# Kernel optimization log

Hardware: AMD Instinct MI355X
Metric: run time of the kernel (lower is better)

The kernel has to match this reference:

```python
import jax, jax.numpy as jnp
import numpy as np

B, S, H = 4, 2048, 2048
E, K = 4, 2
FF = 4 * H  # standard MLP expert expansion


def setup_inputs() -> dict:
    key = jax.random.key(0)
    ks = jax.random.split(key, 5)
    sc = 0.02
    return {
        "hidden_states": jax.random.normal(ks[0], (B, S, H), jnp.float32),
        "w_gate": jax.random.normal(ks[1], (H, E), jnp.float32) * sc,
        "b_gate": jnp.zeros((E,), jnp.float32),
        "w1": jax.random.normal(ks[2], (E, H, FF), jnp.float32) * sc,
        "b1": jnp.zeros((E, FF), jnp.float32),
        "w2": jax.random.normal(ks[3], (E, FF, H), jnp.float32) * sc,
        "b2": jnp.zeros((E, H), jnp.float32),
    }


def reference(hidden_states, w_gate, b_gate, w1, b1, w2, b2):
    # Router: linear gate -> softmax -> top-k, renormalized gate weights
    logits = jnp.einsum("bsh,he->bse", hidden_states, w_gate) + b_gate
    probs = jax.nn.softmax(logits, axis=-1)                       # [B,S,E]
    top_p, top_i = jax.lax.top_k(probs, K)                        # [B,S,K]
    gate_w = top_p / jnp.sum(top_p, axis=-1, keepdims=True)

    # Switch-style load-balancing aux loss
    route = jax.nn.one_hot(top_i, E, dtype=probs.dtype)           # [B,S,K,E]
    frac_tokens = jnp.mean(jnp.sum(route, axis=2) / K, axis=(0, 1))  # [E]
    mean_prob = jnp.mean(probs, axis=(0, 1))                      # [E]
    aux_loss = E * jnp.sum(frac_tokens * mean_prob)

    # Dispatch/combine: small fixed expert count -> loop over experts,
    # dense FFN on all tokens, mask via gate weight (0 for unrouted tokens).
    out = jnp.zeros_like(hidden_states)
    for e in range(E):
        w_e = jnp.sum(gate_w * (top_i == e), axis=-1)             # [B,S]
        h = jax.nn.gelu(jnp.einsum("bsh,hf->bsf", hidden_states, w1[e]) + b1[e])
        y = jnp.einsum("bsf,fh->bsh", h, w2[e]) + b2[e]
        out = out + w_e[..., None] * y
    return out, aux_loss
```

## Files before the change

### kernel.cpp

```cpp
#include <hip/hip_runtime.h>

typedef unsigned short u16;
typedef __attribute__((ext_vector_type(8))) short bf16x8;
typedef __attribute__((ext_vector_type(4))) float f32x4;

#define TOK  8192
#define HD   2048
#define FFD  8192
#define NEXP 4
#define CAPE 4352

__device__ __forceinline__ u16 f2bf(float f){
  unsigned u = __float_as_uint(f);
  u += 0x7fffu + ((u >> 16) & 1u);
  return (u16)(u >> 16);
}

__device__ __forceinline__ float gelu_tanh(float x){
  float u = 0.7978845608028654f * (x + 0.044715f * x * x * x);
  return 0.5f * x * (1.0f + tanhf(u));
}

__device__ __forceinline__ void gload_lds16(const void* g, void* l){
  __builtin_amdgcn_global_load_lds((const __attribute__((address_space(1))) void*)g,
                                   (__attribute__((address_space(3))) void*)l, 16, 0, 0);
}

__device__ __forceinline__ f32x4 mfma_bf16(bf16x8 a, bf16x8 b, f32x4 c){
  asm("v_mfma_f32_16x16x32_bf16 %0, %1, %2, %0" : "+v"(c) : "v"(a), "v"(b));
  return c;
}

__global__ __launch_bounds__(256) void cvt_to_bf16(const float* __restrict__ in,
                                                   u16* __restrict__ out, int n4){
  int i = blockIdx.x * 256 + threadIdx.x;
  if (i >= n4) return;
  float4 v = ((const float4*)in)[i];
  ushort4 o;
  o.x = f2bf(v.x); o.y = f2bf(v.y); o.z = f2bf(v.z); o.w = f2bf(v.w);
  ((ushort4*)out)[i] = o;
}

__global__ __launch_bounds__(256) void transpose_cvt(const float* __restrict__ in,
                                                     u16* __restrict__ out, int R, int C){
  __shared__ u16 t[64][138];
  const int tx = threadIdx.x & 63;
  const int w  = threadIdx.x >> 6;
  const size_t r0 = (size_t)blockIdx.y * 128;
  const size_t c0 = (size_t)blockIdx.x * 64;
  #pragma unroll
  for (int i = 0; i < 32; i++){
    const int r = w * 32 + i;
    t[tx][r] = f2bf(in[(r0 + r) * C + c0 + tx]);
  }
  __syncthreads();
  #pragma unroll
  for (int j = 0; j < 16; j++){
    const int c = j * 4 + w;
    ushort2 o;
    o.x = t[c][2 * tx];
    o.y = t[c][2 * tx + 1];
    *(ushort2*)(out + (c0 + c) * (size_t)R + r0 + 2 * tx) = o;
  }
}

__global__ __launch_bounds__(256) void router_kernel(
    const float* __restrict__ X, const float* __restrict__ wg, const float* __restrict__ bg,
    float* __restrict__ probs, int* __restrict__ topi, float* __restrict__ gatew){
  int t = blockIdx.x;
  const float* x = X + (size_t)t * HD;
  float a0 = 0.f, a1 = 0.f, a2 = 0.f, a3 = 0.f;
  for (int h = threadIdx.x; h < HD; h += 256){
    float xv = x[h];
    float4 w = ((const float4*)wg)[h];
    a0 += xv * w.x; a1 += xv * w.y; a2 += xv * w.z; a3 += xv * w.w;
  }
  __shared__ float red[4][256];
  red[0][threadIdx.x] = a0; red[1][threadIdx.x] = a1;
  red[2][threadIdx.x] = a2; red[3][threadIdx.x] = a3;
  __syncthreads();
  for (int s = 128; s > 0; s >>= 1){
    if (threadIdx.x < (unsigned)s){
      #pragma unroll
      for (int e = 0; e < 4; e++) red[e][threadIdx.x] += red[e][threadIdx.x + s];
    }
    __syncthreads();
  }
  if (threadIdx.x == 0){
    float l[4], p[4];
    #pragma unroll
    for (int e = 0; e < 4; e++) l[e] = red[e][0] + bg[e];
    float mx = fmaxf(fmaxf(l[0], l[1]), fmaxf(l[2], l[3]));
    float s = 0.f;
    #pragma unroll
    for (int e = 0; e < 4; e++){ p[e] = expf(l[e] - mx); s += p[e]; }
    #pragma unroll
    for (int e = 0; e < 4; e++){ p[e] /= s; probs[t * 4 + e] = p[e]; }
    int e0 = 0;
    for (int e = 1; e < 4; e++) if (p[e] > p[e0]) e0 = e;
    int e1 = -1;
    for (int e = 0; e < 4; e++){ if (e == e0) continue; if (e1 < 0 || p[e] > p[e1]) e1 = e; }
    float g = p[e0] + p[e1];
    topi[t * 2] = e0; topi[t * 2 + 1] = e1;
    #pragma unroll
    for (int e = 0; e < 4; e++)
      gatew[(size_t)e * TOK + t] = (e == e0) ? p[e0] / g : (e == e1) ? p[e1] / g : 0.f;
  }
}

__global__ __launch_bounds__(256) void build_lists(const int* __restrict__ topi,
                                                   int* __restrict__ cnt,
                                                   int* __restrict__ lists){
  int t = blockIdx.x * 256 + threadIdx.x;
  if (t >= TOK) return;
  #pragma unroll
  for (int k = 0; k < 2; k++){
    int e = topi[t * 2 + k];
    int p = atomicAdd(cnt + e, 1);
    lists[e * TOK + p] = t;
  }
}

__global__ __launch_bounds__(256) void aux_kernel(const float* __restrict__ probs,
                                                  const int* __restrict__ topi,
                                                  float* __restrict__ out_aux){
  __shared__ float sp[4][256];
  __shared__ float sc[4][256];
  float p[4] = {0,0,0,0}, c[4] = {0,0,0,0};
  for (int t = threadIdx.x; t < TOK; t += 256){
    #pragma unroll
    for (int e = 0; e < 4; e++) p[e] += probs[t * 4 + e];
    c[topi[t * 2]]     += 1.f;
    c[topi[t * 2 + 1]] += 1.f;
  }
  #pragma unroll
  for (int e = 0; e < 4; e++){ sp[e][threadIdx.x] = p[e]; sc[e][threadIdx.x] = c[e]; }
  __syncthreads();
  for (int s = 128; s > 0; s >>= 1){
    if (threadIdx.x < (unsigned)s){
      #pragma unroll
      for (int e = 0; e < 4; e++){
        sp[e][threadIdx.x] += sp[e][threadIdx.x + s];
        sc[e][threadIdx.x] += sc[e][threadIdx.x + s];
      }
    }
    __syncthreads();
  }
  if (threadIdx.x == 0){
    float aux = 0.f;
    #pragma unroll
    for (int e = 0; e < 4; e++)
      aux += (sc[e][0] / (float)(TOK * 2)) * (sp[e][0] / (float)TOK);
    *out_aux = 4.f * aux;
  }
}

template<int EPI, int N, int K>
__global__ __launch_bounds__(256) void gemm_97(
    const u16* __restrict__ A, const u16* __restrict__ BT,
    const int* __restrict__ rowidx, const int* __restrict__ cntp,
    const float* __restrict__ bias,
    u16* __restrict__ Hout,
    const float* __restrict__ gate, float* __restrict__ Cout)
{
  __shared__ __align__(16) u16 As[128 * 64];
  __shared__ __align__(16) u16 Bs[128 * 64];
  const int Mv = *cntp;
  const int gx = gridDim.x, gy = gridDim.y;
  const int orig = blockIdx.x + gx * blockIdx.y;
  const int xcd = orig & 7, rank = orig >> 3;
  const int bxl = rank / gy, by = rank % gy;
  const int bx = xcd * (gx >> 3) + bxl;
  const int browg = by * 128;
  if (browg >= Mv) return;
  const size_t bcol = (size_t)bx * 128;

  const int tid = threadIdx.x, lane = tid & 63, w = tid >> 6;
  const int wr = w >> 1, wc = w & 1;
  const int l8 = lane >> 3;
  const int csw  = ((lane & 7) ^ l8) * 8;
  const int sw   = (lane & 7) * 8;
  const int h8   = ((lane >> 4) & 3) * 8;
  const int colk0 = h8 ^ sw, colk1 = (32 | h8) ^ sw;
  const int r16 = lane & 15;

  const u16* bsrc[4]; int bch[4];
  #pragma unroll
  for (int j = 0; j < 4; j++){
    int rb = j * 32 + w * 8;
    bch[j] = rb * 128;
    bsrc[j] = BT + (bcol + rb + l8) * (size_t)K + csw;
  }
  const u16* asrc[4]; int ach[4];
  #pragma unroll
  for (int q = 0; q < 4; q++){
    int rb = wr * 64 + q * 16 + wc * 8;
    ach[q] = rb * 128;
    int rl = browg + rb + l8;
    int ar;
    if (EPI == 0){
      if (rl > Mv - 1) rl = Mv - 1;
      ar = rowidx[rl];
    } else {
      ar = rl;
    }
    asrc[q] = A + (size_t)ar * K + csw;
  }

  f32x4 acc[4][4];
  #pragma unroll
  for (int m = 0; m < 4; m++)
    #pragma unroll
    for (int n = 0; n < 4; n++) acc[m][n] = (f32x4){0.f, 0.f, 0.f, 0.f};
  bf16x8 bC[8];

  const int NT = K / 64;
  for (int t = 0; t < NT; ++t){
    const size_t ko = (size_t)t * 64;
    __syncthreads();
    #pragma unroll
    for (int j = 0; j < 4; j++) gload_lds16(bsrc[j] + ko, (char*)Bs + bch[j]);
    #pragma unroll
    for (int q = 0; q < 4; q++) gload_lds16(asrc[q] + ko, (char*)As + ach[q]);
    __syncthreads();

    #pragma unroll
    for (int nf = 0; nf < 4; nf++){
      const u16* bp = Bs + (wc * 64 + nf * 16 + r16) * 64;
      bC[nf * 2]     = *(const bf16x8*)(bp + colk0);
      bC[nf * 2 + 1] = *(const bf16x8*)(bp + colk1);
    }
    #pragma unroll
    for (int m = 0; m < 4; m++){
      const u16* ap = As + (wr * 64 + m * 16 + r16) * 64;
      bf16x8 a0 = *(const bf16x8*)(ap + colk0);
      bf16x8 a1 = *(const bf16x8*)(ap + colk1);
      #pragma unroll
      for (int nf = 0; nf < 4; nf++){
        acc[m][nf] = mfma_bf16(a0, bC[nf * 2],     acc[m][nf]);
        acc[m][nf] = mfma_bf16(a1, bC[nf * 2 + 1], acc[m][nf]);
      }
    }
  }

  const int cl = r16, rg = (lane >> 4) * 4;
  const size_t c0 = bcol + wc * 64;
  float bv[4];
  #pragma unroll
  for (int nf = 0; nf < 4; nf++) bv[nf] = bias[c0 + nf * 16 + cl];
  #pragma unroll
  for (int mf = 0; mf < 4; mf++){
    const int rbase = browg + wr * 64 + mf * 16 + rg;
    if (EPI == 0){
      #pragma unroll
      for (int nf = 0; nf < 4; nf++){
        const size_t col = c0 + nf * 16 + cl;
        #pragma unroll
        for (int j = 0; j < 4; j++)
          Hout[(size_t)(rbase + j) * N + col] = f2bf(gelu_tanh(acc[mf][nf][j] + bv[nf]));
      }
    } else {
      int   tok[4]; float gv[4];
      #pragma unroll
      for (int j = 0; j < 4; j++){
        const bool ok = (rbase + j) < Mv;
        tok[j] = ok ? rowidx[rbase + j] : -1;
        gv[j]  = ok ? gate[tok[j]] : 0.f;
      }
      #pragma unroll
      for (int nf = 0; nf < 4; nf++){
        const size_t col = c0 + nf * 16 + cl;
        #pragma unroll
        for (int j = 0; j < 4; j++){
          if (tok[j] >= 0){
            const size_t idx = (size_t)tok[j] * N + col;
            Cout[idx] += gv[j] * (acc[mf][nf][j] + bv[nf]);
          }
        }
      }
    }
  }
}

extern "C" void kernel_launch(void* const* d_in, const int* in_sizes, int n_in,
                              void* d_out, int out_size, void* d_ws, size_t ws_size,
                              hipStream_t stream){
  (void)in_sizes; (void)n_in; (void)ws_size;
  const float* X  = (const float*)d_in[0];
  const float* wg = (const float*)d_in[1];
  const float* bg = (const float*)d_in[2];
  const float* w1 = (const float*)d_in[3];
  const float* b1 = (const float*)d_in[4];
  const float* w2 = (const float*)d_in[5];
  const float* b2 = (const float*)d_in[6];
  float* out = (float*)d_out;

  char* ws = (char*)d_ws;
  size_t off = 0;
  auto alloc = [&](size_t b) -> char* {
    char* p = ws + off;
    off = (off + b + 255) & ~(size_t)255;
    return p;
  };
  u16*   Xb    = (u16*)  alloc((size_t)TOK * HD * 2);
  u16*   W1T   = (u16*)  alloc((size_t)FFD * HD * 2);
  u16*   W2T   = (u16*)  alloc((size_t)HD * FFD * 2);
  float* probs = (float*)alloc((size_t)TOK * 4 * 4);
  int*   topi  = (int*)  alloc((size_t)TOK * 2 * 4);
  float* gatew = (float*)alloc((size_t)NEXP * TOK * 4);
  int*   cnt   = (int*)  alloc((size_t)NEXP * 4);
  int*   lists = (int*)  alloc((size_t)NEXP * TOK * 4);
  u16*   Hb    = (u16*)  alloc((size_t)CAPE * FFD * 2);

  hipMemsetAsync(cnt, 0, NEXP * sizeof(int), stream);
  hipMemsetAsync(out, 0, (size_t)TOK * HD * sizeof(float), stream);

  cvt_to_bf16<<<(TOK * HD / 4 + 255) / 256, 256, 0, stream>>>(X, Xb, TOK * HD / 4);
  router_kernel<<<TOK, 256, 0, stream>>>(X, wg, bg, probs, topi, gatew);
  build_lists<<<TOK / 256, 256, 0, stream>>>(topi, cnt, lists);
  aux_kernel<<<1, 256, 0, stream>>>(probs, topi, out + (out_size - 1));

  for (int e = 0; e < NEXP; ++e){
    transpose_cvt<<<dim3(FFD / 64, HD / 128), 256, 0, stream>>>(
        w1 + (size_t)e * HD * FFD, W1T, HD, FFD);
    transpose_cvt<<<dim3(HD / 64, FFD / 128), 256, 0, stream>>>(
        w2 + (size_t)e * FFD * HD, W2T, FFD, HD);
    gemm_97<0, FFD, HD><<<dim3(FFD / 128, CAPE / 128), 256, 0, stream>>>(
        Xb, W1T, lists + e * TOK, cnt + e, b1 + (size_t)e * FFD,
        Hb, nullptr, nullptr);
    gemm_97<1, HD, FFD><<<dim3(HD / 128, CAPE / 128), 256, 0, stream>>>(
        Hb, W2T, lists + e * TOK, cnt + e, b2 + (size_t)e * HD,
        nullptr, gatew + (size_t)e * TOK, out);
  }
}
```

Measured before the change: 1.694 ms.

## Batch all experts into single grouped GEMM launches with atomic combine

When the workspace is large enough, all expert weights are transposed and converted in one launch each, and both expert GEMMs run as a single launch with the expert on the grid z dimension. Each expert gets its own hidden buffer. The second GEMM accumulates into the output with atomic adds because experts now run concurrently. This removes per-expert launch serialisation and the tail underutilisation of small grids, at the cost of more workspace and atomic traffic on the output. The old per-expert loop remains as a fallback.

```diff
diff --git a/kernel.cpp b/kernel.cpp
--- a/kernel.cpp
+++ b/kernel.cpp
@@ -44,6 +44,8 @@
 __global__ __launch_bounds__(256) void transpose_cvt(const float* __restrict__ in,
                                                      u16* __restrict__ out, int R, int C){
   __shared__ u16 t[64][138];
+  in  += (size_t)blockIdx.z * R * C;
+  out += (size_t)blockIdx.z * R * C;
   const int tx = threadIdx.x & 63;
   const int w  = threadIdx.x >> 6;
   const size_t r0 = (size_t)blockIdx.y * 128;
@@ -155,17 +157,24 @@
   }
 }
 
-template<int EPI, int N, int K>
+template<int EPI, int N, int K, int ATOMIC>
 __global__ __launch_bounds__(256) void gemm_97(
     const u16* __restrict__ A, const u16* __restrict__ BT,
-    const int* __restrict__ rowidx, const int* __restrict__ cntp,
+    const int* __restrict__ lists, const int* __restrict__ cnt,
     const float* __restrict__ bias,
     u16* __restrict__ Hout,
     const float* __restrict__ gate, float* __restrict__ Cout)
 {
   __shared__ __align__(16) u16 As[128 * 64];
   __shared__ __align__(16) u16 Bs[128 * 64];
-  const int Mv = *cntp;
+  const int e = blockIdx.z;
+  const int Mv = cnt[e];
+  const int* rowidx = lists + (size_t)e * TOK;
+  BT   += (size_t)e * N * K;
+  bias += (size_t)e * N;
+  if (EPI == 0) Hout += (size_t)e * CAPE * FFD;
+  else        { A    += (size_t)e * CAPE * FFD; gate += (size_t)e * TOK; }
+
   const int gx = gridDim.x, gy = gridDim.y;
   const int orig = blockIdx.x + gx * blockIdx.y;
   const int xcd = orig & 7, rank = orig >> 3;
@@ -181,7 +190,7 @@
   const int csw  = ((lane & 7) ^ l8) * 8;
   const int sw   = (lane & 7) * 8;
   const int h8   = ((lane >> 4) & 3) * 8;
-  const int colk0 = h8 ^ sw, colk1 = (32 | h8) ^ sw;
+  const int colk0 = h8 ^ sw, colk1 = (32 + h8) ^ sw;
   const int r16 = lane & 15;
 
   const u16* bsrc[4]; int bch[4];
@@ -274,7 +283,9 @@
         for (int j = 0; j < 4; j++){
           if (tok[j] >= 0){
             const size_t idx = (size_t)tok[j] * N + col;
-            Cout[idx] += gv[j] * (acc[mf][nf][j] + bv[nf]);
+            float y = gv[j] * (acc[mf][nf][j] + bv[nf]);
+            if (ATOMIC) atomicAdd(Cout + idx, y);
+            else        Cout[idx] += y;
           }
         }
       }
@@ -285,7 +296,7 @@
 extern "C" void kernel_launch(void* const* d_in, const int* in_sizes, int n_in,
                               void* d_out, int out_size, void* d_ws, size_t ws_size,
                               hipStream_t stream){
-  (void)in_sizes; (void)n_in; (void)ws_size;
+  (void)in_sizes; (void)n_in;
   const float* X  = (const float*)d_in[0];
   const float* wg = (const float*)d_in[1];
   const float* bg = (const float*)d_in[2];
@@ -303,14 +314,17 @@
     return p;
   };
   u16*   Xb    = (u16*)  alloc((size_t)TOK * HD * 2);
-  u16*   W1T   = (u16*)  alloc((size_t)FFD * HD * 2);
-  u16*   W2T   = (u16*)  alloc((size_t)HD * FFD * 2);
   float* probs = (float*)alloc((size_t)TOK * 4 * 4);
   int*   topi  = (int*)  alloc((size_t)TOK * 2 * 4);
   float* gatew = (float*)alloc((size_t)NEXP * TOK * 4);
   int*   cnt   = (int*)  alloc((size_t)NEXP * 4);
   int*   lists = (int*)  alloc((size_t)NEXP * TOK * 4);
-  u16*   Hb    = (u16*)  alloc((size_t)CAPE * FFD * 2);
+  const size_t common = off;
+
+  const size_t w1t_all = (size_t)NEXP * FFD * HD * 2;
+  const size_t w2t_all = (size_t)NEXP * HD * FFD * 2;
+  const size_t hb_all  = (size_t)NEXP * CAPE * FFD * 2;
+  const bool merged = ws_size >= common + w1t_all + w2t_all + hb_all + 1024;
 
   hipMemsetAsync(cnt, 0, NEXP * sizeof(int), stream);
   hipMemsetAsync(out, 0, (size_t)TOK * HD * sizeof(float), stream);
@@ -320,16 +334,31 @@
   build_lists<<<TOK / 256, 256, 0, stream>>>(topi, cnt, lists);
   aux_kernel<<<1, 256, 0, stream>>>(probs, topi, out + (out_size - 1));
 
-  for (int e = 0; e < NEXP; ++e){
-    transpose_cvt<<<dim3(FFD / 64, HD / 128), 256, 0, stream>>>(
-        w1 + (size_t)e * HD * FFD, W1T, HD, FFD);
-    transpose_cvt<<<dim3(HD / 64, FFD / 128), 256, 0, stream>>>(
-        w2 + (size_t)e * FFD * HD, W2T, FFD, HD);
-    gemm_97<0, FFD, HD><<<dim3(FFD / 128, CAPE / 128), 256, 0, stream>>>(
-        Xb, W1T, lists + e * TOK, cnt + e, b1 + (size_t)e * FFD,
-        Hb, nullptr, nullptr);
-    gemm_97<1, HD, FFD><<<dim3(HD / 128, CAPE / 128), 256, 0, stream>>>(
-        Hb, W2T, lists + e * TOK, cnt + e, b2 + (size_t)e * HD,
-        nullptr, gatew + (size_t)e * TOK, out);
-  }
-}
+  if (merged){
+    u16* W1T = (u16*)alloc(w1t_all);
+    u16* W2T = (u16*)alloc(w2t_all);
+    u16* Hb  = (u16*)alloc(hb_all);
+    transpose_cvt<<<dim3(FFD / 64, HD / 128, NEXP), 256, 0, stream>>>(w1, W1T, HD, FFD);
+    transpose_cvt<<<dim3(HD / 64, FFD / 128, NEXP), 256, 0, stream>>>(w2, W2T, FFD, HD);
+    gemm_97<0, FFD, HD, 0><<<dim3(FFD / 128, CAPE / 128, NEXP), 256, 0, stream>>>(
+        Xb, W1T, lists, cnt, b1, Hb, nullptr, nullptr);
+    gemm_97<1, HD, FFD, 1><<<dim3(HD / 128, CAPE / 128, NEXP), 256, 0, stream>>>(
+        Hb, W2T, lists, cnt, b2, nullptr, gatew, out);
+  } else {
+    u16* W1T = (u16*)alloc((size_t)FFD * HD * 2);
+    u16* W2T = (u16*)alloc((size_t)HD * FFD * 2);
+    u16* Hb  = (u16*)alloc((size_t)CAPE * FFD * 2);
+    for (int e = 0; e < NEXP; ++e){
+      transpose_cvt<<<dim3(FFD / 64, HD / 128, 1), 256, 0, stream>>>(
+          w1 + (size_t)e * HD * FFD, W1T, HD, FFD);
+      transpose_cvt<<<dim3(HD / 64, FFD / 128, 1), 256, 0, stream>>>(
+          w2 + (size_t)e * FFD * HD, W2T, FFD, HD);
+      gemm_97<0, FFD, HD, 0><<<dim3(FFD / 128, CAPE / 128, 1), 256, 0, stream>>>(
+          Xb, W1T, lists + e * TOK, cnt + e, b1 + (size_t)e * FFD,
+          Hb, nullptr, nullptr);
+      gemm_97<1, HD, FFD, 0><<<dim3(HD / 128, CAPE / 128, 1), 256, 0, stream>>>(
+          Hb, W2T, lists + e * TOK, cnt + e, b2 + (size_t)e * HD,
+          nullptr, gatew + (size_t)e * TOK, out);
+    }
+  }
+}
```

After: 1.677 ms. No clear change (-1.0%).
